# Kernel tuning notes

Measured on AMD Instinct MI355X. Metric: run time of the kernel, lower is better.

Reference implementation:

```python
import jax, jax.numpy as jnp
import numpy as np

TAU = 0.25
EPS = 1e-6
H, D = 4, 64  # num_heads, out_channels per head


def kernel_feat(data, proj, is_query):
    # softmax_kernel_transformation (Performer positive random features), sigma=1
    d = data.shape[-1]
    x = data * (float(d) ** -0.25)            # data_normalizer = d^{-1/4}
    ratio = float(proj.shape[0]) ** -0.5      # m^{-1/2}
    dd = jnp.einsum('bnhd,md->bnhm', x, proj)
    diag = 0.5 * jnp.sum(x * x, axis=-1, keepdims=True)
    if is_query:
        mx = jnp.max(dd, axis=-1, keepdims=True)
    else:
        mx = jnp.max(dd, axis=(1, -1), keepdims=True)  # max over M then over N
    return ratio * (jnp.exp(dd - diag - mx) + EPS)


def setup_inputs() -> dict:
    key = jax.random.key(0)
    ks = jax.random.split(key, 12)
    N, E, C = 50000, 800000, 128
    M, K = 30, 10
    z = jax.random.normal(ks[0], (1, N, C), dtype=jnp.float32)
    edge_index = jax.random.randint(ks[1], (2, E), 0, N)
    u = jax.random.uniform(ks[2], (N, 1, H, K), dtype=jnp.float32, minval=1e-8, maxval=1.0)
    gumbels = -jnp.log(-jnp.log(u)) / TAU  # Gumbel(0,1)/tau, matches torch -exp().log()/tau
    proj = jax.random.normal(ks[3], (M, D), dtype=jnp.float32)
    s_in = 1.0 / np.sqrt(C)
    s_o = 1.0 / np.sqrt(H * D)
    return {
        'z': z, 'edge_index': edge_index, 'gumbels': gumbels, 'proj': proj,
        'Wq_w': jax.random.normal(ks[4], (C, H * D), dtype=jnp.float32) * s_in,
        'Wq_b': jnp.zeros((H * D,), dtype=jnp.float32),
        'Wk_w': jax.random.normal(ks[5], (C, H * D), dtype=jnp.float32) * s_in,
        'Wk_b': jnp.zeros((H * D,), dtype=jnp.float32),
        'Wv_w': jax.random.normal(ks[6], (C, H * D), dtype=jnp.float32) * s_in,
        'Wv_b': jnp.zeros((H * D,), dtype=jnp.float32),
        'Wo_w': jax.random.normal(ks[7], (H * D, D), dtype=jnp.float32) * s_o,
        'Wo_b': jnp.zeros((D,), dtype=jnp.float32),
    }


def reference(z, edge_index, gumbels, proj, Wq_w, Wq_b, Wk_w, Wk_b, Wv_w, Wv_b, Wo_w, Wo_b):
    B, N, _ = z.shape
    inv_sqrt_tau = 1.0 / jnp.sqrt(jnp.float32(TAU))
    q = ((z @ Wq_w + Wq_b).reshape(B, N, H, D)) * inv_sqrt_tau
    k = ((z @ Wk_w + Wk_b).reshape(B, N, H, D)) * inv_sqrt_tau
    v = (z @ Wv_w + Wv_b).reshape(B, N, H, D)
    qp = jnp.transpose(kernel_feat(q, proj, True), (1, 0, 2, 3))   # [N,B,H,M]
    kp = jnp.transpose(kernel_feat(k, proj, False), (1, 0, 2, 3))  # [N,B,H,M]
    vp = jnp.transpose(v, (1, 0, 2, 3))                            # [N,B,H,D]
    # Gumbel-perturbed keys: [N,B,H,K,M]
    kg = kp[:, :, :, None, :] * jnp.exp(gumbels)[..., None]
    kvs = jnp.einsum('nbhkm,nbhd->bhkmd', kg, vp)
    z_num = jnp.einsum('nbhm,bhkmd->nbhkd', qp, kvs)               # [N,B,H,K,D]
    z_den = jnp.einsum('nbhm,bhkm->nbhk', qp, kg.sum(axis=0))      # [N,B,H,K]
    z_out = jnp.mean(z_num / z_den[..., None], axis=3)             # [N,B,H,D]
    z_out = jnp.transpose(z_out, (1, 0, 2, 3))                     # [B,N,H,D]
    # edge attention weights for edge loss
    start, end = edge_index[0], edge_index[1]
    num = jnp.einsum('ebhm,ebhm->ebh', qp[end], kp[start])
    den = jnp.einsum('nbhm,bhm->nbh', qp, kp.sum(axis=0))[end]
    A_weight = jnp.transpose(num / den, (1, 0, 2))                 # [B,E,H]
    out = z_out.reshape(B, N, H * D) @ Wo_w + Wo_b                 # [B,N,D]
    return out, A_weight
```

## Files before the change

### kernel.cpp

```cpp
#include <hip/hip_runtime.h>
#include <math.h>

#define NH 4
#define ND 64
#define NC 128
#define NHD 256
#define NM 30
#define NK 10
#define EPSF 1e-6f
#define RATIO 0.18257418583505536f
#define QKSCALE 0.7071067811865476f
#define NSEG 48
#define NSEG2 128

typedef float f32x4 __attribute__((ext_vector_type(4)));
typedef short s16x8 __attribute__((ext_vector_type(8)));

__device__ __forceinline__ unsigned f2ord(float f){ unsigned b=__float_as_uint(f); return (b&0x80000000u)?~b:(b|0x80000000u); }
__device__ __forceinline__ float ord2f(unsigned u){ return __uint_as_float((u&0x80000000u)?(u&0x7fffffffu):~u); }
__device__ __forceinline__ ushort f2bf(float f){ unsigned b=__float_as_uint(f); return (ushort)((b + 0x7fffu + ((b>>16)&1u))>>16); }
__device__ __forceinline__ float bf2f(ushort u){ return __uint_as_float(((unsigned)u)<<16); }
__device__ __forceinline__ void bfsplit(float p, unsigned& hi, unsigned& lo){
    unsigned pb = __float_as_uint(p);
    unsigned t  = pb + 0x8000u;
    unsigned hf = t & 0xffff0000u;
    hi = t >> 16;
    lo = __float_as_uint(p - __uint_as_float(hf)) >> 16;
}

__global__ void k_init(unsigned* mxk_u){ if (threadIdx.x < NH) mxk_u[threadIdx.x] = 0u; }

__global__ __launch_bounds__(256) void k_wprep(const float* __restrict__ Wq,
    const float* __restrict__ Wk, const float* __restrict__ Wv,
    ushort* __restrict__ Wt_h, ushort* __restrict__ Wt_l)
{
    int idx = blockIdx.x*256 + threadIdx.x;
    if (idx >= 48*4*64) return;
    int lane = idx & 63, ks = (idx>>6)&3, tile = idx>>8;
    int c = tile*16 + (lane&15);
    int k0 = ks*32 + (lane>>4)*8;
    const float* W; int cc;
    if (c < 256)      { W = Wq; cc = c; }
    else if (c < 512) { W = Wk; cc = c-256; }
    else              { W = Wv; cc = c-512; }
    #pragma unroll
    for (int j=0;j<8;j++){
        float w = W[(size_t)(k0+j)*NHD + cc];
        ushort h = f2bf(w);
        Wt_h[(size_t)idx*8+j] = h;
        Wt_l[(size_t)idx*8+j] = f2bf(w - bf2f(h));
    }
}

__global__ __launch_bounds__(256) void k_wdprep(const float* __restrict__ Wq,
    const float* __restrict__ Wk, const float* __restrict__ proj,
    const float* __restrict__ bq, const float* __restrict__ bk,
    ushort* __restrict__ Wt_h, ushort* __restrict__ Wt_l, float* __restrict__ bd)
{
    __shared__ float wd[16*129];
    int dt = blockIdx.x;
    int tid = threadIdx.x;
    int cl = tid & 15, rc = tid >> 4;
    int cd = dt*16 + cl;
    int isq = (cd < 128);
    int hm = cd & 127;
    int valid = (hm < 120);
    int hh = valid ? hm/30 : 0, m = valid ? hm%30 : 0;
    const float* W = isq ? Wq : Wk;
    const float* prow = proj + (size_t)m*ND;
    #pragma unroll
    for (int rr=0; rr<8; rr++){
        int row = rc*8 + rr;
        float s = 0.f;
        if (valid){
            const float* wr = W + (size_t)row*NHD + hh*64;
            for (int d=0; d<64; d++) s = fmaf(wr[d], prow[d], s);
            s *= QKSCALE;
        }
        wd[cl*129 + row] = s;
    }
    if (tid < 16){
        int cd2 = dt*16 + tid;
        int hm2 = cd2 & 127;
        float s = 0.f;
        if (hm2 < 120){
            int hh2 = hm2/30, m2 = hm2%30;
            const float* bvec = (cd2 < 128) ? bq : bk;
            const float* pr2 = proj + (size_t)m2*ND;
            for (int d=0; d<64; d++) s = fmaf(bvec[hh2*64+d], pr2[d], s);
            s *= QKSCALE;
        }
        bd[cd2] = s;
    }
    __syncthreads();
    int ks = tid >> 6, lane = tid & 63;
    int colL = lane & 15, k0 = ks*32 + (lane>>4)*8;
    unsigned hi[8], lo[8];
    #pragma unroll
    for (int j=0;j<8;j++){
        float v = wd[colL*129 + k0 + j];
        bfsplit(v, hi[j], lo[j]);
    }
    uint4 ph, pl;
    ph.x=hi[0]|(hi[1]<<16); ph.y=hi[2]|(hi[3]<<16); ph.z=hi[4]|(hi[5]<<16); ph.w=hi[6]|(hi[7]<<16);
    pl.x=lo[0]|(lo[1]<<16); pl.y=lo[2]|(lo[3]<<16); pl.z=lo[4]|(lo[5]<<16); pl.w=lo[6]|(lo[7]<<16);
    size_t off = ((size_t)(48+dt)*4 + ks)*64 + lane;
    ((uint4*)Wt_h)[off] = ph;
    ((uint4*)Wt_l)[off] = pl;
}

__global__ __launch_bounds__(256) void k_zfill(float* __restrict__ kpT,
    ushort* __restrict__ vT16, int N, int Npad)
{
    int tail = Npad - N;
    int w1 = 8*Npad, w2 = 128*tail, w3 = 256*tail;
    int idx = blockIdx.x*256 + threadIdx.x;
    if (idx < w1){
        int r = idx / Npad, c = idx % Npad;
        int hh = r>>1, m = 30 + (r&1);
        kpT[((size_t)(hh*32+m))*Npad + c] = 0.f;
    } else if (idx < w1+w2){
        int j = idx - w1; int r = j / tail, c = N + j % tail;
        kpT[(size_t)r*Npad + c] = 0.f;
    } else if (idx < w1+w2+w3){
        int j = idx - w1 - w2; int r = j / tail, c = N + j % tail;
        vT16[(size_t)r*Npad + c] = 0;
    }
}

__global__ __launch_bounds__(256) void k_qkv(
    const float* __restrict__ z,
    const ushort* __restrict__ Wt_h, const ushort* __restrict__ Wt_l,
    const float* __restrict__ bq, const float* __restrict__ bk,
    const float* __restrict__ bv, const float* __restrict__ bd,
    float* __restrict__ qp, ushort* __restrict__ qpe,
    float* __restrict__ dd_k, float* __restrict__ diag_k,
    ushort* __restrict__ vT16, int N, int Npad)
{
    __shared__ float pq[32*132];
    __shared__ float diagq[32*4];
    __shared__ float mxs[32*4];
    int tid = threadIdx.x;
    int n0 = blockIdx.x * 32;
    int w = tid >> 6, lane = tid & 63;
    int l15 = lane & 15, kgrp = lane >> 4;

    s16x8 ah[2][4], al[2][4];
    #pragma unroll
    for (int g=0; g<2; g++){
        int nn = n0 + g*16 + l15; if (nn > N-1) nn = N-1;
        const float* zrow = z + (size_t)nn*NC;
        #pragma unroll
        for (int ks=0;ks<4;ks++){
            f32x4 f0 = *(const f32x4*)(zrow + ks*32 + kgrp*8);
            f32x4 f1 = *(const f32x4*)(zrow + ks*32 + kgrp*8 + 4);
            #pragma unroll
            for (int j=0;j<4;j++){
                float v0 = f0[j]; ushort h0 = f2bf(v0);
                ah[g][ks][j]   = (short)h0; al[g][ks][j]   = (short)f2bf(v0 - bf2f(h0));
                float v1 = f1[j]; ushort h1 = f2bf(v1);
                ah[g][ks][4+j] = (short)h1; al[g][ks][4+j] = (short)f2bf(v1 - bf2f(h1));
            }
        }
    }

    float sq0[4] = {0.f,0.f,0.f,0.f}, sq1[4] = {0.f,0.f,0.f,0.f};
    const uint4* WH = (const uint4*)Wt_h;
    const uint4* WL = (const uint4*)Wt_l;

    for (int nt=0; nt<16; nt++){
        int tile = w*16 + nt;
        f32x4 acc0 = {0.f,0.f,0.f,0.f}, acc1 = {0.f,0.f,0.f,0.f};
        #pragma unroll
        for (int ks=0;ks<4;ks++){
            uint4 bhu = WH[(size_t)(tile*4+ks)*64 + lane];
            uint4 blu = WL[(size_t)(tile*4+ks)*64 + lane];
            s16x8 bh = __builtin_bit_cast(s16x8, bhu);
            s16x8 bl = __builtin_bit_cast(s16x8, blu);
            acc0 = __builtin_amdgcn_mfma_f32_16x16x32_bf16(ah[0][ks], bl, acc0, 0,0,0);
            acc0 = __builtin_amdgcn_mfma_f32_16x16x32_bf16(al[0][ks], bh, acc0, 0,0,0);
            acc0 = __builtin_amdgcn_mfma_f32_16x16x32_bf16(ah[0][ks], bh, acc0, 0,0,0);
            acc1 = __builtin_amdgcn_mfma_f32_16x16x32_bf16(ah[1][ks], bl, acc1, 0,0,0);
            acc1 = __builtin_amdgcn_mfma_f32_16x16x32_bf16(al[1][ks], bh, acc1, 0,0,0);
            acc1 = __builtin_amdgcn_mfma_f32_16x16x32_bf16(ah[1][ks], bh, acc1, 0,0,0);
        }
        int c = tile*16 + l15;
        if (c < 512){
            int ccc = c & 255;
            float bias = (c < 256) ? bq[ccc] : bk[ccc];
            #pragma unroll
            for (int i=0;i<4;i++){
                float x0 = (acc0[i]+bias)*QKSCALE; sq0[i] = fmaf(x0,x0,sq0[i]);
                float x1 = (acc1[i]+bias)*QKSCALE; sq1[i] = fmaf(x1,x1,sq1[i]);
            }
            if ((nt&3)==3){
                int hh = nt>>2;
                #pragma unroll
                for (int i=0;i<4;i++){
                    float s0 = sq0[i], s1 = sq1[i];
                    s0 += __shfl_xor(s0,1); s0 += __shfl_xor(s0,2);
                    s0 += __shfl_xor(s0,4); s0 += __shfl_xor(s0,8);
                    s1 += __shfl_xor(s1,1); s1 += __shfl_xor(s1,2);
                    s1 += __shfl_xor(s1,4); s1 += __shfl_xor(s1,8);
                    if (l15==0){
                        int nd0 = kgrp*4+i, nd1 = 16+kgrp*4+i;
                        if (w==0){ diagq[nd0*4+hh] = 0.5f*s0; diagq[nd1*4+hh] = 0.5f*s1; }
                        else {
                            int na = n0+nd0, nb2 = n0+nd1;
                            if (na < N) diag_k[(size_t)na*4+hh] = 0.5f*s0;
                            if (nb2 < N) diag_k[(size_t)nb2*4+hh] = 0.5f*s1;
                        }
                    }
                    sq0[i]=0.f; sq1[i]=0.f;
                }
            }
        } else if (c < 768){
            int cv = c - 512;
            float bias = bv[cv];
            {
                ushort t0=f2bf(acc0[0]+bias), t1=f2bf(acc0[1]+bias);
                ushort t2=f2bf(acc0[2]+bias), t3=f2bf(acc0[3]+bias);
                int nb = n0 + kgrp*4;
                ushort* dst = &vT16[(size_t)cv*Npad + nb];
                if (nb+4 <= N){ uint2 pk; pk.x=(unsigned)t0|((unsigned)t1<<16); pk.y=(unsigned)t2|((unsigned)t3<<16); *(uint2*)dst=pk; }
                else { if(nb<N)dst[0]=t0; if(nb+1<N)dst[1]=t1; if(nb+2<N)dst[2]=t2; if(nb+3<N)dst[3]=t3; }
            }
            {
                ushort t0=f2bf(acc1[0]+bias), t1=f2bf(acc1[1]+bias);
                ushort t2=f2bf(acc1[2]+bias), t3=f2bf(acc1[3]+bias);
                int nb = n0 + 16 + kgrp*4;
                ushort* dst = &vT16[(size_t)cv*Npad + nb];
                if (nb+4 <= N){ uint2 pk; pk.x=(unsigned)t0|((unsigned)t1<<16); pk.y=(unsigned)t2|((unsigned)t3<<16); *(uint2*)dst=pk; }
                else { if(nb<N)dst[0]=t0; if(nb+1<N)dst[1]=t1; if(nb+2<N)dst[2]=t2; if(nb+3<N)dst[3]=t3; }
            }
        } else {
            int cd = c - 768;
            float bias = bd[cd];
            if (cd < 128){
                #pragma unroll
                for (int i=0;i<4;i++){
                    pq[(kgrp*4+i)*132 + cd]      = acc0[i]+bias;
                    pq[(16+kgrp*4+i)*132 + cd]   = acc1[i]+bias;
                }
            } else {
                int hm = cd - 128;
                if (hm < 120){
                    int hh = hm/30, m = hm%30;
                    size_t base = (size_t)hh*N*NM;
                    #pragma unroll
                    for (int i=0;i<4;i++){
                        int na = n0+kgrp*4+i, nb2 = n0+16+kgrp*4+i;
                        if (na < N)  dd_k[base + (size_t)na*NM + m]  = acc0[i]+bias;
                        if (nb2 < N) dd_k[base + (size_t)nb2*NM + m] = acc1[i]+bias;
                    }
                }
            }
        }
    }
    __syncthreads();

    if (tid < 128){
        int node = tid>>2, hh = tid&3;
        const float* pr = &pq[node*132 + hh*30];
        float mx = -3.0e38f;
        #pragma unroll
        for (int m=0;m<NM;m++) mx = fmaxf(mx, pr[m]);
        mxs[tid] = mx;
    }
    __syncthreads();

    for (int idx = tid; idx < 32*120; idx += 256){
        int node = idx/120, hm = idx%120;
        int n = n0 + node;
        if (n >= N) continue;
        int hh = hm/30;
        float val = RATIO * (__expf(pq[node*132+hm] - diagq[node*4+hh] - mxs[node*4+hh]) + EPSF);
        qp[(size_t)n*120 + hm] = val;
        qpe[(size_t)n*128 + hm] = f2bf(val);
    }
}

__global__ __launch_bounds__(256) void k_maxred(const float* __restrict__ dd_k,
                                                unsigned* __restrict__ mxk_u, int N)
{
    int hh = blockIdx.y;
    size_t len = (size_t)N*NM;
    const float* p = dd_k + (size_t)hh*len;
    float mx = -3.0e38f;
    for (size_t i = (size_t)blockIdx.x*256 + threadIdx.x; i < len; i += (size_t)gridDim.x*256)
        mx = fmaxf(mx, p[i]);
    for (int o=32;o>0;o>>=1) mx = fmaxf(mx, __shfl_down(mx, o));
    __shared__ float wmax[4];
    if ((threadIdx.x & 63) == 0) wmax[threadIdx.x >> 6] = mx;
    __syncthreads();
    if (threadIdx.x == 0) {
        mx = fmaxf(fmaxf(wmax[0],wmax[1]), fmaxf(wmax[2],wmax[3]));
        atomicMax(&mxk_u[hh], f2ord(mx));
    }
}

__global__ __launch_bounds__(256) void k_kp(const float* __restrict__ dd_k,
    const float* __restrict__ diag_k, const unsigned* __restrict__ mxk_u,
    ushort* __restrict__ kpe, float* __restrict__ kpT,
    float* __restrict__ kp_part, int N, int Npad)
{
    __shared__ float tbuf[120*67];
    __shared__ float psum[120];
    int tid = threadIdx.x;
    if (tid < 120) psum[tid] = 0.f;
    float mxk[NH];
    #pragma unroll
    for (int hh=0;hh<NH;hh++) mxk[hh] = ord2f(mxk_u[hh]);
    __syncthreads();
    int n0 = blockIdx.x * 64;
    for (int r = 0; r < 30; r++) {
        int idx = r*256 + tid;
        int nl = idx / 120, hm = idx % 120;
        int n = n0 + nl;
        float val = 0.f;
        if (n < N){
            int hh = hm/30, m = hm%30;
            val = RATIO * (__expf(dd_k[(size_t)hh*N*NM + (size_t)n*NM + m]
                                  - diag_k[(size_t)n*4+hh] - mxk[hh]) + EPSF);
            kpe[(size_t)n*128 + hm] = f2bf(val);
            atomicAdd(&psum[hm], val);
        }
        tbuf[hm*67 + nl] = val;
    }
    __syncthreads();
    for (int i = tid; i < 120*64; i += 256){
        int row = i>>6, cc = i&63;
        int hh = row/30, m = row%30;
        kpT[(size_t)(hh*32+m)*Npad + n0 + cc] = tbuf[row*67 + cc];
    }
    if (tid < 120) kp_part[blockIdx.x*120 + tid] = psum[tid];
}

__global__ __launch_bounds__(256) void k_kpsred(const float* __restrict__ kp_part,
                                                float* __restrict__ kp_sum, int nblk)
{
    int col = blockIdx.x;
    int tid = threadIdx.x;
    float s = 0.f;
    for (int b = tid; b < nblk; b += 256) s += kp_part[(size_t)b*120 + col];
    for (int o=32;o>0;o>>=1) s += __shfl_down(s, o);
    __shared__ float ws_[4];
    if ((tid & 63) == 0) ws_[tid>>6] = s;
    __syncthreads();
    if (tid == 0) kp_sum[col] = ws_[0]+ws_[1]+ws_[2]+ws_[3];
}

__global__ __launch_bounds__(256) void k_eg(const float* __restrict__ gum,
    float* __restrict__ egT, int N, int Npad)
{
    int n0 = blockIdx.x*64;
    for (int i = threadIdx.x; i < 64*40; i += 256){
        int nl = i / 40, hk = i % 40;
        int n = n0 + nl;
        if (n >= Npad) continue;
        float v = (n < N) ? __expf(gum[(size_t)n*40 + hk]) : 0.f;
        egT[(size_t)hk*Npad + n] = v;
    }
}

__global__ __launch_bounds__(256,1) void k_kvs2(const float* __restrict__ kpT,
    const float* __restrict__ egT, const ushort* __restrict__ vT16,
    float* __restrict__ part, int Npad)
{
    int seg = blockIdx.x, hh = blockIdx.y;
    int w = threadIdx.x >> 6, lane = threadIdx.x & 63;
    int l15 = lane & 15, lg = lane >> 4;
    int steps_total = Npad/32;
    int per = (steps_total + NSEG-1)/NSEG;
    int s0 = seg*per, s1 = min(steps_total, s0+per);

    const ushort* vbase = vT16 + (size_t)hh*64*Npad;
    const float* kpbase = kpT + (size_t)hh*32*Npad;
    const float* egbase = egT + (size_t)hh*10*Npad;

    f32x4 acc[5][4];
    #pragma unroll
    for (int mt=0;mt<5;mt++)
        #pragma unroll
        for (int nt=0;nt<4;nt++) acc[mt][nt] = (f32x4){0.f,0.f,0.f,0.f};

    for (int st = s0; st < s1; ++st){
        int n0 = st*32 + lg*8;
        s16x8 bf[4];
        #pragma unroll
        for (int nt=0;nt<4;nt++){
            uint4 u = *(const uint4*)(vbase + (size_t)(nt*16 + l15)*Npad + n0);
            bf[nt] = __builtin_bit_cast(s16x8, u);
        }
        #pragma unroll
        for (int mt=0;mt<5;mt++){
            int r = w*80 + mt*16 + l15;
            int m = r & 31, kk = r >> 5;
            const float* kprow = kpbase + (size_t)m*Npad;
            const float* egrow = egbase + (size_t)kk*Npad;
            f32x4 kp0 = *(const f32x4*)(kprow + n0);
            f32x4 kp1 = *(const f32x4*)(kprow + n0 + 4);
            f32x4 eg0 = *(const f32x4*)(egrow + n0);
            f32x4 eg1 = *(const f32x4*)(egrow + n0 + 4);
            f32x4 pr0 = kp0*eg0, pr1 = kp1*eg1;
            unsigned hi[8], lo[8];
            #pragma unroll
            for (int j=0;j<4;j++){
                bfsplit(pr0[j], hi[j], lo[j]);
                bfsplit(pr1[j], hi[4+j], lo[4+j]);
            }
            uint4 ahu, alu;
            ahu.x = hi[0]|(hi[1]<<16); ahu.y = hi[2]|(hi[3]<<16);
            ahu.z = hi[4]|(hi[5]<<16); ahu.w = hi[6]|(hi[7]<<16);
            alu.x = lo[0]|(lo[1]<<16); alu.y = lo[2]|(lo[3]<<16);
            alu.z = lo[4]|(lo[5]<<16); alu.w = lo[6]|(lo[7]<<16);
            s16x8 ah = __builtin_bit_cast(s16x8, ahu);
            s16x8 al = __builtin_bit_cast(s16x8, alu);
            #pragma unroll
            for (int nt=0;nt<4;nt++){
                acc[mt][nt] = __builtin_amdgcn_mfma_f32_16x16x32_bf16(al, bf[nt], acc[mt][nt], 0,0,0);
                acc[mt][nt] = __builtin_amdgcn_mfma_f32_16x16x32_bf16(ah, bf[nt], acc[mt][nt], 0,0,0);
            }
        }
    }
    float* dst = part + ((size_t)hh*NSEG + seg)*20480;
    #pragma unroll
    for (int mt=0;mt<5;mt++)
        #pragma unroll
        for (int nt=0;nt<4;nt++)
            #pragma unroll
            for (int i=0;i<4;i++){
                int rr = w*80 + mt*16 + lg*4 + i;
                dst[rr*64 + nt*16 + l15] = acc[mt][nt][i];
            }
}

__global__ void k_kvsred2(const float* __restrict__ part, float* __restrict__ kvs){
    int o = blockIdx.x*256 + threadIdx.x;
    if (o >= 76800) return;
    int hh = o / 19200, r = o % 19200;
    int km = r >> 6, d = r & 63;
    int kk = km / 30, m = km % 30;
    size_t base = (size_t)hh*NSEG*20480 + (size_t)(kk*32+m)*64 + d;
    float s = 0.f;
    for (int sg=0; sg<NSEG; sg++) s += part[base + (size_t)sg*20480];
    kvs[o] = s;
}

__global__ __launch_bounds__(320) void k_kgp(const float* __restrict__ kpT,
    const float* __restrict__ egT, float* __restrict__ kg_part, int Npad)
{
    int s2 = blockIdx.x, hh = blockIdx.y;
    int t = threadIdx.x;
    int kk = t >> 5, m = t & 31;
    int len = Npad / NSEG2;
    int n0 = s2*len;
    float acc = 0.f;
    if (kk < NK && m < NM){
        const f32x4* kr = (const f32x4*)(kpT + ((size_t)(hh*32+m))*Npad + n0);
        const f32x4* er = (const f32x4*)(egT + ((size_t)(hh*10+kk))*Npad + n0);
        for (int i=0;i<len/4;i++){
            f32x4 a = kr[i], b = er[i];
            acc = fmaf(a.x, b.x, acc); acc = fmaf(a.y, b.y, acc);
            acc = fmaf(a.z, b.z, acc); acc = fmaf(a.w, b.w, acc);
        }
    }
    kg_part[((size_t)hh*NSEG2 + s2)*320 + t] = acc;
}

__global__ void k_kgred2(const float* __restrict__ kg_part, float* __restrict__ kg_sum){
    int o = blockIdx.x*64 + threadIdx.x;
    if (o >= 1200) return;
    int hh = o / 300, r = o % 300;
    int kk = r / 30, m = r % 30;
    float s = 0.f;
    for (int i=0;i<NSEG2;i++) s += kg_part[((size_t)hh*NSEG2 + i)*320 + kk*32 + m];
    kg_sum[o] = s;
}

__global__ __launch_bounds__(256) void k_wkprep(const float* __restrict__ kvs,
    const float* __restrict__ Wo, ushort* __restrict__ WKf_h, ushort* __restrict__ WKf_l)
{
    __shared__ float kv_s[30*65];
    __shared__ float wo_s[64*64];
    __shared__ float wks[32*64];
    int ks = blockIdx.x;
    int h = ks/10, kq = ks%10;
    int tid = threadIdx.x;
    for (int i=tid;i<1920;i+=256){ int m=i>>6, d=i&63; kv_s[m*65+d] = kvs[(size_t)h*19200 + (size_t)(kq*30)*64 + i]; }
    for (int i=tid;i<4096;i+=256) wo_s[i] = Wo[(size_t)h*64*64 + i];
    __syncthreads();
    int m = tid>>3, c0 = (tid&7)*8;
    float acc[8] = {0,0,0,0,0,0,0,0};
    if (m < 30){
        for (int d=0; d<64; d++){
            float kv = kv_s[m*65+d];
            const float* wr = &wo_s[d*64 + c0];
            #pragma unroll
            for (int j=0;j<8;j++) acc[j] = fmaf(kv, wr[j], acc[j]);
        }
    }
    #pragma unroll
    for (int j=0;j<8;j++) wks[m*64 + c0 + j] = acc[j];
    __syncthreads();
    int nt = tid>>6, lane = tid&63, l15 = lane&15, lg = lane>>4;
    unsigned hi[8], lo[8];
    #pragma unroll
    for (int jj=0;jj<8;jj++){
        float v = wks[(lg*8+jj)*64 + nt*16 + l15];
        bfsplit(v, hi[jj], lo[jj]);
    }
    uint4 ph, pl;
    ph.x = hi[0]|(hi[1]<<16); ph.y = hi[2]|(hi[3]<<16); ph.z = hi[4]|(hi[5]<<16); ph.w = hi[6]|(hi[7]<<16);
    pl.x = lo[0]|(lo[1]<<16); pl.y = lo[2]|(lo[3]<<16); pl.z = lo[4]|(lo[5]<<16); pl.w = lo[6]|(lo[7]<<16);
    size_t off = ((size_t)ks*4 + nt)*64 + lane;
    ((uint4*)WKf_h)[off] = ph;
    ((uint4*)WKf_l)[off] = pl;
}

__global__ __launch_bounds__(256) void k_zo(const float* __restrict__ qp,
    const ushort* __restrict__ WKf_h, const ushort* __restrict__ WKf_l,
    const float* __restrict__ kg_sum, const float* __restrict__ kp_sum,
    const float* __restrict__ Wob, ushort* __restrict__ qpe,
    float* __restrict__ out, int N)
{
    __shared__ float kg_s[1200];
    __shared__ float kps_s[120];
    __shared__ uint4 bs[2][2][256];
    int tid = threadIdx.x;
    int w = tid>>6, lane = tid&63, l15 = lane&15, lg = lane>>4;
    int n0 = blockIdx.x*64;
    int n = n0 + w*16 + l15;
    bool nv = (n < N);
    int nc = nv ? n : (N-1);

    for (int i=tid;i<1200;i+=256) kg_s[i] = kg_sum[i];
    if (tid < 120) kps_s[tid] = kp_sum[tid];
    {
        const uint4* sH = (const uint4*)WKf_h;
        const uint4* sL = (const uint4*)WKf_l;
        bs[0][0][tid] = sH[tid];
        bs[0][1][tid] = sL[tid];
    }

    float qA[4][8];
    const float* qrow = qp + (size_t)nc*120;
    #pragma unroll
    for (int h=0;h<4;h++)
      #pragma unroll
      for (int jj=0;jj<8;jj++){
        int m = lg*8+jj;
        qA[h][jj] = (m<30) ? qrow[h*30+m] : 0.f;
      }
    __syncthreads();

    #pragma unroll
    for (int h=0;h<4;h++){
      float p = 0.f;
      #pragma unroll
      for (int jj=0;jj<8;jj++){
        int m = lg*8+jj;
        if (m<30) p = fmaf(qA[h][jj], kps_s[h*30+m], p);
      }
      p += __shfl_xor(p,16);
      p += __shfl_xor(p,32);
      if (lg==0 && nv) ((float*)qpe)[(size_t)n*64 + 60 + h] = p;
    }

    f32x4 acc[4];
    #pragma unroll
    for (int nt=0;nt<4;nt++) acc[nt] = (f32x4){0.f,0.f,0.f,0.f};

    #pragma unroll
    for (int h=0;h<4;h++){
      for (int kq=0;kq<10;kq++){
        int ks = h*10+kq;
        int buf = ks&1;
        if (ks < 39){
            const uint4* sH = (const uint4*)WKf_h + (size_t)(ks+1)*256;
            const uint4* sL = (const uint4*)WKf_l + (size_t)(ks+1)*256;
            bs[buf^1][0][tid] = sH[tid];
            bs[buf^1][1][tid] = sL[tid];
        }
        float p = 0.f;
        #pragma unroll
        for (int jj=0;jj<8;jj++){
          int m = lg*8+jj;
          if (m<30) p = fmaf(qA[h][jj], kg_s[h*300 + kq*30 + m], p);
        }
        p += __shfl_xor(p,16);
        p += __shfl_xor(p,32);
        float sc = 0.1f / p;
        unsigned hi[8], lo[8];
        #pragma unroll
        for (int jj=0;jj<8;jj++) bfsplit(qA[h][jj]*sc, hi[jj], lo[jj]);
        uint4 ahu, alu;
        ahu.x = hi[0]|(hi[1]<<16); ahu.y = hi[2]|(hi[3]<<16);
        ahu.z = hi[4]|(hi[5]<<16); ahu.w = hi[6]|(hi[7]<<16);
        alu.x = lo[0]|(lo[1]<<16); alu.y = lo[2]|(lo[3]<<16);
        alu.z = lo[4]|(lo[5]<<16); alu.w = lo[6]|(lo[7]<<16);
        s16x8 ah = __builtin_bit_cast(s16x8, ahu);
        s16x8 al = __builtin_bit_cast(s16x8, alu);
        #pragma unroll
        for (int nt=0;nt<4;nt++){
            s16x8 bh = __builtin_bit_cast(s16x8, bs[buf][0][nt*64+lane]);
            s16x8 bl = __builtin_bit_cast(s16x8, bs[buf][1][nt*64+lane]);
            acc[nt] = __builtin_amdgcn_mfma_f32_16x16x32_bf16(ah, bl, acc[nt], 0,0,0);
            acc[nt] = __builtin_amdgcn_mfma_f32_16x16x32_bf16(al, bh, acc[nt], 0,0,0);
            acc[nt] = __builtin_amdgcn_mfma_f32_16x16x32_bf16(ah, bh, acc[nt], 0,0,0);
        }
        __syncthreads();
      }
    }

    #pragma unroll
    for (int nt=0;nt<4;nt++){
        float bias = Wob[nt*16 + l15];
        #pragma unroll
        for (int i=0;i<4;i++){
            int node = n0 + w*16 + lg*4 + i;
            if (node < N) out[(size_t)node*64 + nt*16 + l15] = acc[nt][i] + bias;
        }
    }
}

__global__ __launch_bounds__(256) void k_edge(const int* __restrict__ ei,
    const ushort* __restrict__ qpe, const ushort* __restrict__ kpe,
    float* __restrict__ A, int E)
{
    int tid = threadIdx.x;
    int e = blockIdx.x*64 + (tid>>2);
    int sub = tid & 3;
    if (e >= E) return;
    int s = ei[e], t = ei[E + e];
    const uint4* rq = (const uint4*)(qpe + (size_t)t*128) + sub*4;
    const uint4* rk = (const uint4*)(kpe + (size_t)s*128) + sub*4;
    float numA = 0.f, numB = 0.f;
    int bndw = 15 - sub;
    #define PROC(au,bu,wi) { \
        float a0=__uint_as_float((au)<<16),        b0=__uint_as_float((bu)<<16); \
        float a1=__uint_as_float((au)&0xffff0000u),b1=__uint_as_float((bu)&0xffff0000u); \
        float p = fmaf(a0,b0, a1*b1); \
        if ((wi) < bndw) numA += p; else if (sub < 3) numB += p; }
    #pragma unroll
    for (int j=0;j<4;j++){
        uint4 a = rq[j], b = rk[j];
        PROC(a.x, b.x, j*4+0)
        PROC(a.y, b.y, j*4+1)
        PROC(a.z, b.z, j*4+2)
        PROC(a.w, b.w, j*4+3)
    }
    #undef PROC
    int lane = tid & 63;
    float nbIn = __shfl(numB, (lane > 0) ? (lane-1) : 0);
    float num = numA + ((sub > 0) ? nbIn : 0.f);
    float dnv = ((const float*)(qpe + (size_t)t*128))[60 + sub];
    A[(size_t)e*4 + sub] = num / dnv;
}

extern "C" void kernel_launch(void* const* d_in, const int* in_sizes, int n_in,
                              void* d_out, int out_size, void* d_ws, size_t ws_size,
                              hipStream_t stream)
{
    const float* z    = (const float*)d_in[0];
    const int*   ei   = (const int*)d_in[1];
    const float* gum  = (const float*)d_in[2];
    const float* proj = (const float*)d_in[3];
    const float* Wq   = (const float*)d_in[4];
    const float* bq   = (const float*)d_in[5];
    const float* Wk   = (const float*)d_in[6];
    const float* bk   = (const float*)d_in[7];
    const float* Wv   = (const float*)d_in[8];
    const float* bv   = (const float*)d_in[9];
    const float* Wo   = (const float*)d_in[10];
    const float* Wob  = (const float*)d_in[11];
    int N = in_sizes[0] / NC;
    int E = in_sizes[1] / 2;
    int Npad = (N + 511) & ~511;

    float* ws = (float*)d_ws;
    size_t o = 0;
    #define ALIGN64 o = (o + 63) & ~(size_t)63;
    float* qp       = ws + o; o += (size_t)N*120;
    ALIGN64
    float* vbuf     = ws + o; o += (size_t)N*NHD;
    ALIGN64
    float* dd_k     = ws + o; o += (size_t)NH*N*NM;
    float* egT      = dd_k;
    float* kvs_part = dd_k + (size_t)40*Npad;
    ALIGN64
    float* diag_k   = ws + o; o += (size_t)N*4;
    unsigned* mxk_u = (unsigned*)(ws + o); o += 4;
    ALIGN64
    int nkb = (N+63)/64;
    float* kp_part  = ws + o; o += (size_t)nkb*120;
    float* kp_sum   = ws + o; o += 120;
    ALIGN64
    float* kg_part  = ws + o; o += (size_t)NH*NSEG2*320;
    float* kvs      = ws + o; o += 76800;
    float* kg_sum   = ws + o; o += 1200;
    ALIGN64
    ushort* qpe     = (ushort*)(ws + o); o += (size_t)N*64;
    ALIGN64
    ushort* kpe     = (ushort*)(ws + o); o += (size_t)N*64;
    ALIGN64
    ushort* Wt_h    = (ushort*)(ws + o); o += 64*4*64*8/2;
    ALIGN64
    ushort* Wt_l    = (ushort*)(ws + o); o += 64*4*64*8/2;
    ALIGN64
    float* bd       = ws + o; o += 256;
    ALIGN64
    float* kpT      = ws + o; o += (size_t)128*Npad;
    ALIGN64
    ushort* WKf_h   = (ushort*)(ws + o); o += 40*4*64*8/2;
    ALIGN64
    ushort* WKf_l   = (ushort*)(ws + o); o += 40*4*64*8/2;
    ushort* vT16    = (ushort*)vbuf;

    float* out = (float*)d_out;
    float* A   = out + (size_t)N*ND;

    k_wprep<<<dim3(48), dim3(256), 0, stream>>>(Wq, Wk, Wv, Wt_h, Wt_l);
    k_wdprep<<<dim3(16), dim3(256), 0, stream>>>(Wq, Wk, proj, bq, bk, Wt_h, Wt_l, bd);
    k_init<<<dim3(1), dim3(64), 0, stream>>>(mxk_u);
    {
        int tail = Npad - N;
        int zwork = 8*Npad + (128+256)*tail;
        k_zfill<<<dim3((zwork+255)/256), dim3(256), 0, stream>>>(kpT, vT16, N, Npad);
    }
    k_qkv<<<dim3((N+31)/32), dim3(256), 0, stream>>>(z, Wt_h, Wt_l, bq, bk, bv, bd,
                                                     qp, qpe, dd_k, diag_k, vT16, N, Npad);
    k_maxred<<<dim3(48,4), dim3(256), 0, stream>>>(dd_k, mxk_u, N);
    k_kp<<<dim3(nkb), dim3(256), 0, stream>>>(dd_k, diag_k, mxk_u, kpe, kpT, kp_part, N, Npad);
    k_kpsred<<<dim3(120), dim3(256), 0, stream>>>(kp_part, kp_sum, nkb);
    k_eg<<<dim3(Npad/64), dim3(256), 0, stream>>>(gum, egT, N, Npad);
    k_kvs2<<<dim3(NSEG, NH), dim3(256), 0, stream>>>(kpT, egT, vT16, kvs_part, Npad);
    k_kgp<<<dim3(NSEG2, NH), dim3(320), 0, stream>>>(kpT, egT, kg_part, Npad);
    k_kvsred2<<<dim3(300), dim3(256), 0, stream>>>(kvs_part, kvs);
    k_kgred2<<<dim3(19), dim3(64), 0, stream>>>(kg_part, kg_sum);
    k_wkprep<<<dim3(40), dim3(256), 0, stream>>>(kvs, Wo, WKf_h, WKf_l);
    k_zo<<<dim3((N+63)/64), dim3(256), 0, stream>>>(qp, WKf_h, WKf_l, kg_sum, kp_sum,
                                                    Wob, qpe, out, N);
    k_edge<<<dim3((E+63)/64), dim3(256), 0, stream>>>(ei, qpe, kpe, A, E);
}
```

Before: 482.0 us.

## Fuse prep/reduction launches, fold key max into QKV, prefetch interleaved weights

Merges the weight-prep, projection-prep, zero-fill and max-init kernels into one launch. It also merges the kp-sum with gumbel-exp, and the two partial-sum reductions, so fewer small kernels are launched. The separate pass that re-reads dd_k for the global key max is removed; k_qkv now computes per-head maxima in registers and issues an atomicMax per block. The hi/lo bf16 weight tiles are interleaved into one buffer and double-buffered in registers across output tiles. The risks are extra register pressure in k_qkv and atomic contention from about 1500 blocks.

```diff
diff --git a/kernel.cpp b/kernel.cpp
--- a/kernel.cpp
+++ b/kernel.cpp
@@ -28,114 +28,116 @@
     lo = __float_as_uint(p - __uint_as_float(hf)) >> 16;
 }
 
-__global__ void k_init(unsigned* mxk_u){ if (threadIdx.x < NH) mxk_u[threadIdx.x] = 0u; }
-
-__global__ __launch_bounds__(256) void k_wprep(const float* __restrict__ Wq,
+__global__ __launch_bounds__(256) void k_prep(const float* __restrict__ Wq,
     const float* __restrict__ Wk, const float* __restrict__ Wv,
-    ushort* __restrict__ Wt_h, ushort* __restrict__ Wt_l)
-{
-    int idx = blockIdx.x*256 + threadIdx.x;
-    if (idx >= 48*4*64) return;
-    int lane = idx & 63, ks = (idx>>6)&3, tile = idx>>8;
-    int c = tile*16 + (lane&15);
-    int k0 = ks*32 + (lane>>4)*8;
-    const float* W; int cc;
-    if (c < 256)      { W = Wq; cc = c; }
-    else if (c < 512) { W = Wk; cc = c-256; }
-    else              { W = Wv; cc = c-512; }
-    #pragma unroll
-    for (int j=0;j<8;j++){
-        float w = W[(size_t)(k0+j)*NHD + cc];
-        ushort h = f2bf(w);
-        Wt_h[(size_t)idx*8+j] = h;
-        Wt_l[(size_t)idx*8+j] = f2bf(w - bf2f(h));
-    }
-}
-
-__global__ __launch_bounds__(256) void k_wdprep(const float* __restrict__ Wq,
-    const float* __restrict__ Wk, const float* __restrict__ proj,
-    const float* __restrict__ bq, const float* __restrict__ bk,
-    ushort* __restrict__ Wt_h, ushort* __restrict__ Wt_l, float* __restrict__ bd)
+    const float* __restrict__ proj, const float* __restrict__ bq,
+    const float* __restrict__ bk, ushort* __restrict__ Wt,
+    float* __restrict__ bd, float* __restrict__ kpT, ushort* __restrict__ vT16,
+    unsigned* __restrict__ mxk_u, int zwork, int N, int Npad)
 {
     __shared__ float wd[16*129];
-    int dt = blockIdx.x;
+    int b = blockIdx.x;
     int tid = threadIdx.x;
-    int cl = tid & 15, rc = tid >> 4;
-    int cd = dt*16 + cl;
-    int isq = (cd < 128);
-    int hm = cd & 127;
-    int valid = (hm < 120);
-    int hh = valid ? hm/30 : 0, m = valid ? hm%30 : 0;
-    const float* W = isq ? Wq : Wk;
-    const float* prow = proj + (size_t)m*ND;
-    #pragma unroll
-    for (int rr=0; rr<8; rr++){
-        int row = rc*8 + rr;
-        float s = 0.f;
-        if (valid){
-            const float* wr = W + (size_t)row*NHD + hh*64;
-            for (int d=0; d<64; d++) s = fmaf(wr[d], prow[d], s);
-            s *= QKSCALE;
-        }
-        wd[cl*129 + row] = s;
-    }
-    if (tid < 16){
-        int cd2 = dt*16 + tid;
-        int hm2 = cd2 & 127;
-        float s = 0.f;
-        if (hm2 < 120){
-            int hh2 = hm2/30, m2 = hm2%30;
-            const float* bvec = (cd2 < 128) ? bq : bk;
-            const float* pr2 = proj + (size_t)m2*ND;
-            for (int d=0; d<64; d++) s = fmaf(bvec[hh2*64+d], pr2[d], s);
-            s *= QKSCALE;
-        }
-        bd[cd2] = s;
-    }
-    __syncthreads();
-    int ks = tid >> 6, lane = tid & 63;
-    int colL = lane & 15, k0 = ks*32 + (lane>>4)*8;
-    unsigned hi[8], lo[8];
-    #pragma unroll
-    for (int j=0;j<8;j++){
-        float v = wd[colL*129 + k0 + j];
-        bfsplit(v, hi[j], lo[j]);
-    }
-    uint4 ph, pl;
-    ph.x=hi[0]|(hi[1]<<16); ph.y=hi[2]|(hi[3]<<16); ph.z=hi[4]|(hi[5]<<16); ph.w=hi[6]|(hi[7]<<16);
-    pl.x=lo[0]|(lo[1]<<16); pl.y=lo[2]|(lo[3]<<16); pl.z=lo[4]|(lo[5]<<16); pl.w=lo[6]|(lo[7]<<16);
-    size_t off = ((size_t)(48+dt)*4 + ks)*64 + lane;
-    ((uint4*)Wt_h)[off] = ph;
-    ((uint4*)Wt_l)[off] = pl;
-}
-
-__global__ __launch_bounds__(256) void k_zfill(float* __restrict__ kpT,
-    ushort* __restrict__ vT16, int N, int Npad)
-{
-    int tail = Npad - N;
-    int w1 = 8*Npad, w2 = 128*tail, w3 = 256*tail;
-    int idx = blockIdx.x*256 + threadIdx.x;
-    if (idx < w1){
-        int r = idx / Npad, c = idx % Npad;
-        int hh = r>>1, m = 30 + (r&1);
-        kpT[((size_t)(hh*32+m))*Npad + c] = 0.f;
-    } else if (idx < w1+w2){
-        int j = idx - w1; int r = j / tail, c = N + j % tail;
-        kpT[(size_t)r*Npad + c] = 0.f;
-    } else if (idx < w1+w2+w3){
-        int j = idx - w1 - w2; int r = j / tail, c = N + j % tail;
-        vT16[(size_t)r*Npad + c] = 0;
+    uint4* WT = (uint4*)Wt;
+    if (b < 48){
+        int idx = b*256 + tid;
+        int lane = idx & 63, ks = (idx>>6)&3, tile = idx>>8;
+        int c = tile*16 + (lane&15);
+        int k0 = ks*32 + (lane>>4)*8;
+        const float* W; int cc;
+        if (c < 256)      { W = Wq; cc = c; }
+        else if (c < 512) { W = Wk; cc = c-256; }
+        else              { W = Wv; cc = c-512; }
+        ushort h[8], l[8];
+        #pragma unroll
+        for (int j=0;j<8;j++){
+            float w = W[(size_t)(k0+j)*NHD + cc];
+            h[j] = f2bf(w);
+            l[j] = f2bf(w - bf2f(h[j]));
+        }
+        uint4 ph, pl;
+        ph.x=(unsigned)h[0]|((unsigned)h[1]<<16); ph.y=(unsigned)h[2]|((unsigned)h[3]<<16);
+        ph.z=(unsigned)h[4]|((unsigned)h[5]<<16); ph.w=(unsigned)h[6]|((unsigned)h[7]<<16);
+        pl.x=(unsigned)l[0]|((unsigned)l[1]<<16); pl.y=(unsigned)l[2]|((unsigned)l[3]<<16);
+        pl.z=(unsigned)l[4]|((unsigned)l[5]<<16); pl.w=(unsigned)l[6]|((unsigned)l[7]<<16);
+        WT[(size_t)idx*2]   = ph;
+        WT[(size_t)idx*2+1] = pl;
+    } else if (b < 64){
+        int dt = b - 48;
+        int cl = tid & 15, rc = tid >> 4;
+        int cd = dt*16 + cl;
+        int isq = (cd < 128);
+        int hm = cd & 127;
+        int valid = (hm < 120);
+        int hh = valid ? hm/30 : 0, m = valid ? hm%30 : 0;
+        const float* W = isq ? Wq : Wk;
+        const float* prow = proj + (size_t)m*ND;
+        #pragma unroll
+        for (int rr=0; rr<8; rr++){
+            int row = rc*8 + rr;
+            float s = 0.f;
+            if (valid){
+                const float* wr = W + (size_t)row*NHD + hh*64;
+                for (int d=0; d<64; d++) s = fmaf(wr[d], prow[d], s);
+                s *= QKSCALE;
+            }
+            wd[cl*129 + row] = s;
+        }
+        if (tid < 16){
+            int cd2 = dt*16 + tid;
+            int hm2 = cd2 & 127;
+            float s = 0.f;
+            if (hm2 < 120){
+                int hh2 = hm2/30, m2 = hm2%30;
+                const float* bvec = (cd2 < 128) ? bq : bk;
+                const float* pr2 = proj + (size_t)m2*ND;
+                for (int d=0; d<64; d++) s = fmaf(bvec[hh2*64+d], pr2[d], s);
+                s *= QKSCALE;
+            }
+            bd[cd2] = s;
+        }
+        __syncthreads();
+        int ks = tid >> 6, lane = tid & 63;
+        int colL = lane & 15, k0 = ks*32 + (lane>>4)*8;
+        unsigned hi[8], lo[8];
+        #pragma unroll
+        for (int j=0;j<8;j++){
+            float v = wd[colL*129 + k0 + j];
+            bfsplit(v, hi[j], lo[j]);
+        }
+        uint4 ph, pl;
+        ph.x=hi[0]|(hi[1]<<16); ph.y=hi[2]|(hi[3]<<16); ph.z=hi[4]|(hi[5]<<16); ph.w=hi[6]|(hi[7]<<16);
+        pl.x=lo[0]|(lo[1]<<16); pl.y=lo[2]|(lo[3]<<16); pl.z=lo[4]|(lo[5]<<16); pl.w=lo[6]|(lo[7]<<16);
+        size_t off = ((size_t)(48+dt)*4 + ks)*64 + lane;
+        WT[off*2]   = ph;
+        WT[off*2+1] = pl;
+    } else {
+        int idx = (b-64)*256 + tid;
+        int tail = Npad - N;
+        int w1 = 8*Npad, w2 = 128*tail, w3 = 256*tail;
+        if (idx < w1){
+            int r = idx / Npad, c = idx % Npad;
+            int hh = r>>1, m = 30 + (r&1);
+            kpT[((size_t)(hh*32+m))*Npad + c] = 0.f;
+        } else if (idx < w1+w2){
+            int j = idx - w1; int r = j / tail, c = N + j % tail;
+            kpT[(size_t)r*Npad + c] = 0.f;
+        } else if (idx < w1+w2+w3){
+            int j = idx - w1 - w2; int r = j / tail, c = N + j % tail;
+            vT16[(size_t)r*Npad + c] = 0;
+        } else if (idx >= zwork && idx < zwork + 4){
+            mxk_u[idx - zwork] = 0u;
+        }
     }
 }
 
 __global__ __launch_bounds__(256) void k_qkv(
-    const float* __restrict__ z,
-    const ushort* __restrict__ Wt_h, const ushort* __restrict__ Wt_l,
+    const float* __restrict__ z, const ushort* __restrict__ Wt,
     const float* __restrict__ bq, const float* __restrict__ bk,
     const float* __restrict__ bv, const float* __restrict__ bd,
     float* __restrict__ qp, ushort* __restrict__ qpe,
     float* __restrict__ dd_k, float* __restrict__ diag_k,
-    ushort* __restrict__ vT16, int N, int Npad)
+    ushort* __restrict__ vT16, unsigned* __restrict__ mxk_u, int N, int Npad)
 {
     __shared__ float pq[32*132];
     __shared__ float diagq[32*4];
@@ -144,6 +146,7 @@
     int n0 = blockIdx.x * 32;
     int w = tid >> 6, lane = tid & 63;
     int l15 = lane & 15, kgrp = lane >> 4;
+    const uint4* WT = (const uint4*)Wt;
 
     s16x8 ah[2][4], al[2][4];
     #pragma unroll
@@ -165,16 +168,32 @@
     }
 
     float sq0[4] = {0.f,0.f,0.f,0.f}, sq1[4] = {0.f,0.f,0.f,0.f};
-    const uint4* WH = (const uint4*)Wt_h;
-    const uint4* WL = (const uint4*)Wt_l;
-
+    float mk0=-3.0e38f, mk1=-3.0e38f, mk2=-3.0e38f, mk3=-3.0e38f;
+    int tile0 = w*16;
+
+    uint4 bhA[4], blA[4], bhB[4], blB[4];
+    #pragma unroll
+    for (int ks=0;ks<4;ks++){
+        int off = ((tile0*4+ks)*64 + lane)*2;
+        bhA[ks] = WT[off]; blA[ks] = WT[off+1];
+    }
+
+    #pragma unroll
     for (int nt=0; nt<16; nt++){
-        int tile = w*16 + nt;
+        int tile = tile0 + nt;
+        if (nt < 15){
+            #pragma unroll
+            for (int ks=0;ks<4;ks++){
+                int off = (((tile+1)*4+ks)*64 + lane)*2;
+                if (nt & 1){ bhA[ks] = WT[off]; blA[ks] = WT[off+1]; }
+                else       { bhB[ks] = WT[off]; blB[ks] = WT[off+1]; }
+            }
+        }
         f32x4 acc0 = {0.f,0.f,0.f,0.f}, acc1 = {0.f,0.f,0.f,0.f};
         #pragma unroll
         for (int ks=0;ks<4;ks++){
-            uint4 bhu = WH[(size_t)(tile*4+ks)*64 + lane];
-            uint4 blu = WL[(size_t)(tile*4+ks)*64 + lane];
+            uint4 bhu = (nt & 1) ? bhB[ks] : bhA[ks];
+            uint4 blu = (nt & 1) ? blB[ks] : blA[ks];
             s16x8 bh = __builtin_bit_cast(s16x8, bhu);
             s16x8 bl = __builtin_bit_cast(s16x8, blu);
             acc0 = __builtin_amdgcn_mfma_f32_16x16x32_bf16(ah[0][ks], bl, acc0, 0,0,0);
@@ -253,8 +272,28 @@
                         if (na < N)  dd_k[base + (size_t)na*NM + m]  = acc0[i]+bias;
                         if (nb2 < N) dd_k[base + (size_t)nb2*NM + m] = acc1[i]+bias;
                     }
+                    float vm = fmaxf(fmaxf(fmaxf(acc0[0],acc0[1]),fmaxf(acc0[2],acc0[3])),
+                                     fmaxf(fmaxf(acc1[0],acc1[1]),fmaxf(acc1[2],acc1[3]))) + bias;
+                    mk0 = (hh==0) ? fmaxf(mk0, vm) : mk0;
+                    mk1 = (hh==1) ? fmaxf(mk1, vm) : mk1;
+                    mk2 = (hh==2) ? fmaxf(mk2, vm) : mk2;
+                    mk3 = (hh==3) ? fmaxf(mk3, vm) : mk3;
                 }
             }
+        }
+    }
+
+    if (w == 3){
+        #pragma unroll
+        for (int h=0; h<4; h++){
+            float v = (h==0)?mk0:(h==1)?mk1:(h==2)?mk2:mk3;
+            v = fmaxf(v, __shfl_xor(v,1));
+            v = fmaxf(v, __shfl_xor(v,2));
+            v = fmaxf(v, __shfl_xor(v,4));
+            v = fmaxf(v, __shfl_xor(v,8));
+            v = fmaxf(v, __shfl_xor(v,16));
+            v = fmaxf(v, __shfl_xor(v,32));
+            if (lane == 0) atomicMax(&mxk_u[h], f2ord(v));
         }
     }
     __syncthreads();
@@ -277,25 +316,6 @@
         float val = RATIO * (__expf(pq[node*132+hm] - diagq[node*4+hh] - mxs[node*4+hh]) + EPSF);
         qp[(size_t)n*120 + hm] = val;
         qpe[(size_t)n*128 + hm] = f2bf(val);
-    }
-}
-
-__global__ __launch_bounds__(256) void k_maxred(const float* __restrict__ dd_k,
-                                                unsigned* __restrict__ mxk_u, int N)
-{
-    int hh = blockIdx.y;
-    size_t len = (size_t)N*NM;
-    const float* p = dd_k + (size_t)hh*len;
-    float mx = -3.0e38f;
-    for (size_t i = (size_t)blockIdx.x*256 + threadIdx.x; i < len; i += (size_t)gridDim.x*256)
-        mx = fmaxf(mx, p[i]);
-    for (int o=32;o>0;o>>=1) mx = fmaxf(mx, __shfl_down(mx, o));
-    __shared__ float wmax[4];
-    if ((threadIdx.x & 63) == 0) wmax[threadIdx.x >> 6] = mx;
-    __syncthreads();
-    if (threadIdx.x == 0) {
-        mx = fmaxf(fmaxf(wmax[0],wmax[1]), fmaxf(wmax[2],wmax[3]));
-        atomicMax(&mxk_u[hh], f2ord(mx));
     }
 }
 
@@ -336,30 +356,29 @@
     if (tid < 120) kp_part[blockIdx.x*120 + tid] = psum[tid];
 }
 
-__global__ __launch_bounds__(256) void k_kpsred(const float* __restrict__ kp_part,
-                                                float* __restrict__ kp_sum, int nblk)
-{
-    int col = blockIdx.x;
+__global__ __launch_bounds__(256) void k_mid(const float* __restrict__ kp_part,
+    float* __restrict__ kp_sum, int nblk,
+    const float* __restrict__ gum, float* __restrict__ egT, int N, int Npad)
+{
+    __shared__ float ws_[4];
+    int b = blockIdx.x;
     int tid = threadIdx.x;
-    float s = 0.f;
-    for (int b = tid; b < nblk; b += 256) s += kp_part[(size_t)b*120 + col];
-    for (int o=32;o>0;o>>=1) s += __shfl_down(s, o);
-    __shared__ float ws_[4];
-    if ((tid & 63) == 0) ws_[tid>>6] = s;
-    __syncthreads();
-    if (tid == 0) kp_sum[col] = ws_[0]+ws_[1]+ws_[2]+ws_[3];
-}
-
-__global__ __launch_bounds__(256) void k_eg(const float* __restrict__ gum,
-    float* __restrict__ egT, int N, int Npad)
-{
-    int n0 = blockIdx.x*64;
-    for (int i = threadIdx.x; i < 64*40; i += 256){
-        int nl = i / 40, hk = i % 40;
-        int n = n0 + nl;
-        if (n >= Npad) continue;
-        float v = (n < N) ? __expf(gum[(size_t)n*40 + hk]) : 0.f;
-        egT[(size_t)hk*Npad + n] = v;
+    if (b < 120){
+        float s = 0.f;
+        for (int bb = tid; bb < nblk; bb += 256) s += kp_part[(size_t)bb*120 + b];
+        for (int o=32;o>0;o>>=1) s += __shfl_down(s, o);
+        if ((tid & 63) == 0) ws_[tid>>6] = s;
+        __syncthreads();
+        if (tid == 0) kp_sum[b] = ws_[0]+ws_[1]+ws_[2]+ws_[3];
+    } else {
+        int n0 = (b-120)*64;
+        for (int i = tid; i < 64*40; i += 256){
+            int nl = i / 40, hk = i % 40;
+            int n = n0 + nl;
+            if (n >= Npad) continue;
+            float v = (n < N) ? __expf(gum[(size_t)n*40 + hk]) : 0.f;
+            egT[(size_t)hk*Npad + n] = v;
+        }
     }
 }
 
@@ -435,18 +454,6 @@
             }
 }
 
-__global__ void k_kvsred2(const float* __restrict__ part, float* __restrict__ kvs){
-    int o = blockIdx.x*256 + threadIdx.x;
-    if (o >= 76800) return;
-    int hh = o / 19200, r = o % 19200;
-    int km = r >> 6, d = r & 63;
-    int kk = km / 30, m = km % 30;
-    size_t base = (size_t)hh*NSEG*20480 + (size_t)(kk*32+m)*64 + d;
-    float s = 0.f;
-    for (int sg=0; sg<NSEG; sg++) s += part[base + (size_t)sg*20480];
-    kvs[o] = s;
-}
-
 __global__ __launch_bounds__(320) void k_kgp(const float* __restrict__ kpT,
     const float* __restrict__ egT, float* __restrict__ kg_part, int Npad)
 {
@@ -468,14 +475,30 @@
     kg_part[((size_t)hh*NSEG2 + s2)*320 + t] = acc;
 }
 
-__global__ void k_kgred2(const float* __restrict__ kg_part, float* __restrict__ kg_sum){
-    int o = blockIdx.x*64 + threadIdx.x;
-    if (o >= 1200) return;
-    int hh = o / 300, r = o % 300;
-    int kk = r / 30, m = r % 30;
-    float s = 0.f;
-    for (int i=0;i<NSEG2;i++) s += kg_part[((size_t)hh*NSEG2 + i)*320 + kk*32 + m];
-    kg_sum[o] = s;
+__global__ __launch_bounds__(256) void k_red(const float* __restrict__ part,
+    float* __restrict__ kvs, const float* __restrict__ kg_part,
+    float* __restrict__ kg_sum)
+{
+    int b = blockIdx.x, tid = threadIdx.x;
+    if (b < 300){
+        int o = b*256 + tid;
+        if (o >= 76800) return;
+        int hh = o / 19200, r = o % 19200;
+        int km = r >> 6, d = r & 63;
+        int kk = km / 30, m = km % 30;
+        size_t base = (size_t)hh*NSEG*20480 + (size_t)(kk*32+m)*64 + d;
+        float s = 0.f;
+        for (int sg=0; sg<NSEG; sg++) s += part[base + (size_t)sg*20480];
+        kvs[o] = s;
+    } else {
+        int o = (b-300)*256 + tid;
+        if (o >= 1200) return;
+        int hh = o / 300, r = o % 300;
+        int kk = r / 30, m = r % 30;
+        float s = 0.f;
+        for (int i=0;i<NSEG2;i++) s += kg_part[((size_t)hh*NSEG2 + i)*320 + kk*32 + m];
+        kg_sum[o] = s;
+    }
 }
 
 __global__ __launch_bounds__(256) void k_wkprep(const float* __restrict__ kvs,
@@ -704,9 +727,7 @@
     ALIGN64
     ushort* kpe     = (ushort*)(ws + o); o += (size_t)N*64;
     ALIGN64
-    ushort* Wt_h    = (ushort*)(ws + o); o += 64*4*64*8/2;
-    ALIGN64
-    ushort* Wt_l    = (ushort*)(ws + o); o += 64*4*64*8/2;
+    ushort* Wt      = (ushort*)(ws + o); o += (size_t)64*4*64*8;
     ALIGN64
     float* bd       = ws + o; o += 256;
     ALIGN64
@@ -720,24 +741,21 @@
     float* out = (float*)d_out;
     float* A   = out + (size_t)N*ND;
 
-    k_wprep<<<dim3(48), dim3(256), 0, stream>>>(Wq, Wk, Wv, Wt_h, Wt_l);
-    k_wdprep<<<dim3(16), dim3(256), 0, stream>>>(Wq, Wk, proj, bq, bk, Wt_h, Wt_l, bd);
-    k_init<<<dim3(1), dim3(64), 0, stream>>>(mxk_u);
-    {
-        int tail = Npad - N;
-        int zwork = 8*Npad + (128+256)*tail;
-        k_zfill<<<dim3((zwork+255)/256), dim3(256), 0, stream>>>(kpT, vT16, N, Npad);
-    }
-    k_qkv<<<dim3((N+31)/32), dim3(256), 0, stream>>>(z, Wt_h, Wt_l, bq, bk, bv, bd,
-                                                     qp, qpe, dd_k, diag_k, vT16, N, Npad);
-    k_maxred<<<dim3(48,4), dim3(256), 0, stream>>>(dd_k, mxk_u, N);
+    int tail = Npad - N;
+    int zwork = 8*Npad + (128+256)*tail;
+    int zb = (zwork + 4 + 255)/256;
+    k_prep<<<dim3(64 + zb), dim3(256), 0, stream>>>(Wq, Wk, Wv, proj, bq, bk,
+                                                    Wt, bd, kpT, vT16, mxk_u,
+                                                    zwork, N, Npad);
+    k_qkv<<<dim3((N+31)/32), dim3(256), 0, stream>>>(z, Wt, bq, bk, bv, bd,
+                                                     qp, qpe, dd_k, diag_k, vT16,
+                                                     mxk_u, N, Npad);
     k_kp<<<dim3(nkb), dim3(256), 0, stream>>>(dd_k, diag_k, mxk_u, kpe, kpT, kp_part, N, Npad);
-    k_kpsred<<<dim3(120), dim3(256), 0, stream>>>(kp_part, kp_sum, nkb);
-    k_eg<<<dim3(Npad/64), dim3(256), 0, stream>>>(gum, egT, N, Npad);
+    k_mid<<<dim3(120 + Npad/64), dim3(256), 0, stream>>>(kp_part, kp_sum, nkb,
+                                                         gum, egT, N, Npad);
     k_kvs2<<<dim3(NSEG, NH), dim3(256), 0, stream>>>(kpT, egT, vT16, kvs_part, Npad);
     k_kgp<<<dim3(NSEG2, NH), dim3(320), 0, stream>>>(kpT, egT, kg_part, Npad);
-    k_kvsred2<<<dim3(300), dim3(256), 0, stream>>>(kvs_part, kvs);
-    k_kgred2<<<dim3(19), dim3(64), 0, stream>>>(kg_part, kg_sum);
+    k_red<<<dim3(305), dim3(256), 0, stream>>>(kvs_part, kvs, kg_part, kg_sum);
     k_wkprep<<<dim3(40), dim3(256), 0, stream>>>(kvs, Wo, WKf_h, WKf_l);
     k_zo<<<dim3((N+63)/64), dim3(256), 0, stream>>>(qp, WKf_h, WKf_l, kg_sum, kp_sum,
                                                     Wob, qpe, out, N);
```

Measured after the change: 453.2 us. 6.0% less time.
